# Kernel tuning notes

Measured on AMD Instinct MI355X. Metric: run time of the kernel, lower is better.

Reference implementation:

```python
import jax, jax.numpy as jnp
import numpy as np

N = 100000
E = 1600000
IN = 128
HID = 128
OUT = 64


def sage_conv(x, src, dst, deg_inv, W_l, b_l, W_r):
    # PyG SAGEConv (mean aggr): out = lin_l(mean_{j in N(i)} x_j) + lin_r(x_i)
    msgs = x[src]                                   # [E, F] gather
    agg = jax.ops.segment_sum(msgs, dst, num_segments=N)  # [N, F]
    agg = agg * deg_inv[:, None]                    # mean
    return agg @ W_l + b_l + x @ W_r


def setup_inputs() -> dict:
    key = jax.random.key(0)
    ks = jax.random.split(key, 9)
    x = jax.random.normal(ks[0], (N, IN), dtype=jnp.float32)
    edge_index = jax.random.randint(ks[1], (2, E), 0, N, dtype=jnp.int64)
    s = 1.0 / np.sqrt(IN)
    W1l = jax.random.uniform(ks[2], (IN, HID), jnp.float32, -s, s)
    b1 = jax.random.uniform(ks[3], (HID,), jnp.float32, -s, s)
    W1r = jax.random.uniform(ks[4], (IN, HID), jnp.float32, -s, s)
    s2 = 1.0 / np.sqrt(HID)
    W2l = jax.random.uniform(ks[5], (HID, HID), jnp.float32, -s2, s2)
    b2 = jax.random.uniform(ks[6], (HID,), jnp.float32, -s2, s2)
    W2r = jax.random.uniform(ks[7], (HID, HID), jnp.float32, -s2, s2)
    kl1, kl2 = jax.random.split(ks[8])
    Wlin = jax.random.uniform(kl1, (HID, OUT), jnp.float32, -s2, s2)
    blin = jax.random.uniform(kl2, (OUT,), jnp.float32, -s2, s2)
    return {"x": x, "edge_index": edge_index, "W1l": W1l, "b1": b1, "W1r": W1r,
            "W2l": W2l, "b2": b2, "W2r": W2r, "Wlin": Wlin, "blin": blin}


def reference(x, edge_index, W1l, b1, W1r, W2l, b2, W2r, Wlin, blin):
    src, dst = edge_index[0], edge_index[1]
    deg = jax.ops.segment_sum(jnp.ones((E,), jnp.float32), dst, num_segments=N)
    deg_inv = 1.0 / jnp.maximum(deg, 1.0)
    h = sage_conv(x, src, dst, deg_inv, W1l, b1, W1r)
    h = jax.nn.relu(h)
    # dropout: training=False -> identity
    h2 = sage_conv(h, src, dst, deg_inv, W2l, b2, W2r)
    h = jax.nn.relu(h + h2)
    return h @ Wlin + blin
```

## Files before the change

kernel.cpp:

```cpp
#include <hip/hip_runtime.h>
#include <hip/hip_bf16.h>
#include <cstdint>

#define NND 100000
#define NED 1600000
#define FIN 128
#define FOUT 64

#define NBLK 512
#define EPB (NED / NBLK)
#define NBUCK 256
#define BSH 9
#define BNODES 512
#define HTN (NBUCK * NBLK)

typedef __bf16 bf16x8 __attribute__((ext_vector_type(8)));
typedef float f32x4 __attribute__((ext_vector_type(4)));

static __device__ inline unsigned short f2bf(float f) {
    unsigned int u = __builtin_bit_cast(unsigned int, f);
    unsigned int r = (u + 0x7fffu + ((u >> 16) & 1u)) >> 16;
    return (unsigned short)r;
}
static __device__ inline float bflo(unsigned int v) {
    return __builtin_bit_cast(float, v << 16);
}
static __device__ inline float bfhi(unsigned int v) {
    return __builtin_bit_cast(float, v & 0xffff0000u);
}
static __device__ inline float bf1(unsigned short u) {
    return __builtin_bit_cast(float, (unsigned int)u << 16);
}

static __device__ inline void pack_one(const float* __restrict__ W,
                                       unsigned short* __restrict__ out,
                                       int NTtot, int c_local, int nt,
                                       int chunkOff, int ncols, int lane) {
    int k = c_local * 32 + (lane >> 4) * 8;
    int n = nt * 16 + (lane & 15);
    unsigned short t[8];
#pragma unroll
    for (int j = 0; j < 8; j++) t[j] = f2bf(W[(size_t)(k + j) * ncols + n]);
    uint4 u;
    u.x = t[0] | ((unsigned)t[1] << 16);
    u.y = t[2] | ((unsigned)t[3] << 16);
    u.z = t[4] | ((unsigned)t[5] << 16);
    u.w = t[6] | ((unsigned)t[7] << 16);
    *(uint4*)&out[((size_t)((c_local + chunkOff) * NTtot + nt) * 64 + lane) * 8] = u;
}

__global__ __launch_bounds__(256) void k_hist_cast(
        const int* __restrict__ dst, int* __restrict__ histT,
        const float* __restrict__ x, unsigned int* __restrict__ xb,
        const float* W1l, const float* W1r, const float* W2l,
        const float* W2r, const float* Wlin,
        unsigned short* p1, unsigned short* p2, unsigned short* ph) {
    __shared__ int hist[NBUCK];
    const int tid = threadIdx.x, blk = blockIdx.x;
    hist[tid] = 0;
    __syncthreads();
    const int e0 = blk * EPB, e1 = e0 + EPB;
    for (int i = e0 + tid; i < e1; i += 256)
        atomicAdd(&hist[dst[i] >> BSH], 1);
    __syncthreads();
    histT[tid * NBLK + blk] = hist[tid];
    if (blk < 144 && tid < 64) {
        int b = blk, lane = tid;
        if (b < 32)       pack_one(W1l, p1, 8, b >> 3, b & 7, 0, 128, lane);
        else if (b < 64)  { b -= 32; pack_one(W1r, p1, 8, b >> 3, b & 7, 4, 128, lane); }
        else if (b < 96)  { b -= 64; pack_one(W2l, p2, 8, b >> 3, b & 7, 0, 128, lane); }
        else if (b < 128) { b -= 96; pack_one(W2r, p2, 8, b >> 3, b & 7, 4, 128, lane); }
        else              { b -= 128; pack_one(Wlin, ph, 4, b >> 2, b & 3, 0, 64, lane); }
    }
    const int total2 = NND * 64;
    for (int i = blk * 256 + tid; i < total2; i += NBLK * 256) {
        float2 v = ((const float2*)x)[i];
        xb[i] = (unsigned int)f2bf(v.x) | ((unsigned int)f2bf(v.y) << 16);
    }
}

__global__ __launch_bounds__(1024) void g_scan1(const int* __restrict__ in,
                                                int* __restrict__ psum, int n) {
    __shared__ int red[1024];
    int tid = threadIdx.x;
    int i = blockIdx.x * 1024 + tid;
    red[tid] = (i < n) ? in[i] : 0;
    __syncthreads();
#pragma unroll
    for (int off = 512; off > 0; off >>= 1) {
        if (tid < off) red[tid] += red[tid + off];
        __syncthreads();
    }
    if (tid == 0) psum[blockIdx.x] = red[0];
}

__global__ __launch_bounds__(128) void g_scan2(int* __restrict__ psum, int nb) {
    int tid = threadIdx.x;
    int d = (tid < nb) ? psum[tid] : 0;
    int v = d;
#pragma unroll
    for (int off = 1; off < 64; off <<= 1) {
        int u = __shfl_up(v, off, 64);
        if ((tid & 63) >= off) v += u;
    }
    __shared__ int ws[2];
    if ((tid & 63) == 63) ws[tid >> 6] = v;
    __syncthreads();
    int base = (tid >= 64) ? ws[0] : 0;
    if (tid < nb) psum[tid] = base + v - d;
}

__global__ __launch_bounds__(1024) void g_scan3(const int* __restrict__ in,
                                                const int* __restrict__ psum,
                                                int* __restrict__ out, int n) {
    int tid = threadIdx.x;
    int i = blockIdx.x * 1024 + tid;
    int d = (i < n) ? in[i] : 0;
    int v = d;
#pragma unroll
    for (int off = 1; off < 64; off <<= 1) {
        int u = __shfl_up(v, off, 64);
        if ((tid & 63) >= off) v += u;
    }
    __shared__ int wsum[16];
    int wid = tid >> 6;
    if ((tid & 63) == 63) wsum[wid] = v;
    __syncthreads();
    if (tid < 16) {
        int w = wsum[tid];
#pragma unroll
        for (int off = 1; off < 16; off <<= 1) {
            int u = __shfl_up(w, off, 64);
            if (tid >= off) w += u;
        }
        wsum[tid] = w;
    }
    __syncthreads();
    int base = psum[blockIdx.x] + (wid ? wsum[wid - 1] : 0);
    if (i < n) out[i] = base + v - d;
}

__global__ __launch_bounds__(256) void k_scatter(const int* __restrict__ src,
                                                 const int* __restrict__ dst,
                                                 const int* __restrict__ sh,
                                                 uint2* __restrict__ eS) {
    __shared__ int cur[NBUCK];
    const int tid = threadIdx.x, blk = blockIdx.x;
    cur[tid] = sh[tid * NBLK + blk];
    __syncthreads();
    const int e0 = blk * EPB, e1 = e0 + EPB;
    for (int i = e0 + tid; i < e1; i += 256) {
        int d = dst[i];
        int pos = atomicAdd(&cur[d >> BSH], 1);
        eS[pos] = make_uint2((unsigned)src[i], (unsigned)(d & (BNODES - 1)));
    }
}

__global__ __launch_bounds__(1024) void k_bucket(const uint2* __restrict__ eS,
                                                 const int* __restrict__ sh,
                                                 int* __restrict__ csr,
                                                 int* __restrict__ offs,
                                                 float* __restrict__ dinv, int n) {
    __shared__ int cnt[BNODES];
    __shared__ int loc[BNODES];
    const int b = blockIdx.x, tid = threadIdx.x;
    const int base = sh[b * NBLK];
    const int end = (b == NBUCK - 1) ? NED : sh[(b + 1) * NBLK];
    if (tid < BNODES) cnt[tid] = 0;
    __syncthreads();
    for (int i = base + tid; i < end; i += 1024)
        atomicAdd(&cnt[eS[i].y], 1);
    __syncthreads();
    if (tid < BNODES) loc[tid] = cnt[tid];
    __syncthreads();
#pragma unroll
    for (int off = 1; off < BNODES; off <<= 1) {
        int v = 0;
        if (tid < BNODES && tid >= off) v = loc[tid - off];
        __syncthreads();
        if (tid < BNODES) loc[tid] += v;
        __syncthreads();
    }
    int node = b * BNODES + tid;
    int myExcl = 0;
    if (tid < BNODES) {
        myExcl = loc[tid] - cnt[tid];
        if (node < n) {
            offs[node] = base + myExcl;
            dinv[node] = 1.0f / fmaxf((float)cnt[tid], 1.0f);
        }
    }
    __syncthreads();
    if (tid < BNODES) cnt[tid] = base + myExcl;
    __syncthreads();
    for (int i = base + tid; i < end; i += 1024) {
        uint2 e = eS[i];
        int slot = atomicAdd(&cnt[e.y], 1);
        csr[slot] = (int)e.x;
    }
    if (b == 0 && tid == 0) offs[n] = NED;
}

#define ACC8(v) do { \
    acc[0].x += bflo((v).x); acc[0].y += bfhi((v).x); \
    acc[1].x += bflo((v).y); acc[1].y += bfhi((v).y); \
    acc[2].x += bflo((v).z); acc[2].y += bfhi((v).z); \
    acc[3].x += bflo((v).w); acc[3].y += bfhi((v).w); } while (0)

__global__ __launch_bounds__(256) void k_aggb(const uint4* __restrict__ feat4,
                                              const int* __restrict__ offs,
                                              const int* __restrict__ csr,
                                              const float* __restrict__ dinv,
                                              uint4* __restrict__ out4, int n) {
    int node = blockIdx.x * 4 + (threadIdx.x >> 6);
    if (node >= n) return;
    int lane = threadIdx.x & 63;
    int grp = lane >> 4;
    int ch = lane & 15;
    int beg = offs[node], end = offs[node + 1];
    int deg = end - beg;

    float2 acc[4];
#pragma unroll
    for (int j = 0; j < 4; j++) acc[j] = make_float2(0.f, 0.f);

    int i = beg;
    int fullEnd = beg + (deg & ~15);
    for (; i < fullEnd; i += 16) {
        int s0 = csr[i + grp];
        int s1 = csr[i + 4 + grp];
        int s2 = csr[i + 8 + grp];
        int s3 = csr[i + 12 + grp];
        uint4 v0 = feat4[(size_t)s0 * 16 + ch];
        uint4 v1 = feat4[(size_t)s1 * 16 + ch];
        uint4 v2 = feat4[(size_t)s2 * 16 + ch];
        uint4 v3 = feat4[(size_t)s3 * 16 + ch];
        ACC8(v0); ACC8(v1); ACC8(v2); ACC8(v3);
    }
    if (i < end) {
#pragma unroll
        for (int g = 0; g < 4; g++) {
            int e = i + g * 4 + grp;
            bool p = e < end;
            int s = csr[p ? e : beg];
            uint4 v = feat4[(size_t)s * 16 + ch];
            if (p) { ACC8(v); }
        }
    }
#pragma unroll
    for (int j = 0; j < 4; j++) {
        acc[j].x += __shfl_xor(acc[j].x, 16);
        acc[j].y += __shfl_xor(acc[j].y, 16);
        acc[j].x += __shfl_xor(acc[j].x, 32);
        acc[j].y += __shfl_xor(acc[j].y, 32);
    }
    if (grp == 0) {
        float di = dinv[node];
        uint4 o;
        o.x = (unsigned)f2bf(acc[0].x * di) | ((unsigned)f2bf(acc[0].y * di) << 16);
        o.y = (unsigned)f2bf(acc[1].x * di) | ((unsigned)f2bf(acc[1].y * di) << 16);
        o.z = (unsigned)f2bf(acc[2].x * di) | ((unsigned)f2bf(acc[2].y * di) << 16);
        o.w = (unsigned)f2bf(acc[3].x * di) | ((unsigned)f2bf(acc[3].y * di) << 16);
        out4[(size_t)node * 16 + ch] = o;
    }
}

template <int NT, int KCH, bool TWO, bool RELU, bool RESID, bool HEAD, bool OUTBF>
__global__ __launch_bounds__(256) void k_mfma(const unsigned short* __restrict__ P,
                                              const unsigned short* __restrict__ Q,
                                              const unsigned short* __restrict__ Wp,
                                              const float* __restrict__ bias,
                                              const unsigned short* __restrict__ resid,
                                              const unsigned short* __restrict__ Wp2,
                                              const float* __restrict__ bias2,
                                              void* __restrict__ outv, int n) {
    const int lane = threadIdx.x & 63;
    const int wave = threadIdx.x >> 6;
    const int quad = lane >> 4;
    const int row0 = blockIdx.x * 64 + wave * 16;
    int rowA = row0 + (lane & 15);
    if (rowA >= n) rowA = n - 1;

    f32x4 acc[NT];
#pragma unroll
    for (int t = 0; t < NT; t++) acc[t] = (f32x4){0.f, 0.f, 0.f, 0.f};

#pragma unroll
    for (int c = 0; c < KCH; c++) {
        const unsigned short* Abase = (TWO && c >= KCH / 2) ? Q : P;
        const int kk = (TWO ? (c & (KCH / 2 - 1)) : c) * 32 + quad * 8;
        bf16x8 a = *(const bf16x8*)&Abase[(size_t)rowA * 128 + kk];
#pragma unroll
        for (int t = 0; t < NT; t++) {
            bf16x8 b = *(const bf16x8*)&Wp[(size_t)((c * NT + t) * 64 + lane) * 8];
            acc[t] = __builtin_amdgcn_mfma_f32_16x16x32_bf16(a, b, acc[t], 0, 0, 0);
        }
    }

    const int col = lane & 15;
    if (!HEAD) {
#pragma unroll
        for (int t = 0; t < NT; t++) {
            float bv = bias[t * 16 + col];
#pragma unroll
            for (int r = 0; r < 4; r++) {
                int row = row0 + quad * 4 + r;
                if (row < n) {
                    float v = acc[t][r] + bv;
                    if (RESID) v += bf1(resid[(size_t)row * 128 + t * 16 + col]);
                    if (RELU) v = fmaxf(v, 0.f);
                    if (OUTBF)
                        ((unsigned short*)outv)[(size_t)row * (NT * 16) + t * 16 + col] = f2bf(v);
                    else
                        ((float*)outv)[(size_t)row * (NT * 16) + t * 16 + col] = v;
                }
            }
        }
    } else {
        __shared__ __align__(16) unsigned short sT[4][16 * 136];
#pragma unroll
        for (int t = 0; t < NT; t++) {
            float bv = bias[t * 16 + col];
#pragma unroll
            for (int r = 0; r < 4; r++) {
                int row = row0 + quad * 4 + r;
                int rr = row < n ? row : n - 1;
                float v = acc[t][r] + bv;
                if (RESID) v += bf1(resid[(size_t)rr * 128 + t * 16 + col]);
                if (RELU) v = fmaxf(v, 0.f);
                sT[wave][(quad * 4 + r) * 136 + t * 16 + col] = f2bf(v);
            }
        }
        f32x4 hacc[4];
#pragma unroll
        for (int t = 0; t < 4; t++) hacc[t] = (f32x4){0.f, 0.f, 0.f, 0.f};
#pragma unroll
        for (int c = 0; c < 4; c++) {
            bf16x8 a = *(const bf16x8*)&sT[wave][(lane & 15) * 136 + c * 32 + quad * 8];
#pragma unroll
            for (int t = 0; t < 4; t++) {
                bf16x8 b = *(const bf16x8*)&Wp2[(size_t)((c * 4 + t) * 64 + lane) * 8];
                hacc[t] = __builtin_amdgcn_mfma_f32_16x16x32_bf16(a, b, hacc[t], 0, 0, 0);
            }
        }
#pragma unroll
        for (int t = 0; t < 4; t++) {
            float bv = bias2[t * 16 + col];
#pragma unroll
            for (int r = 0; r < 4; r++) {
                int row = row0 + quad * 4 + r;
                if (row < n)
                    ((float*)outv)[(size_t)row * 64 + t * 16 + col] = hacc[t][r] + bv;
            }
        }
    }
}

extern "C" void kernel_launch(void* const* d_in, const int* in_sizes, int n_in,
                              void* d_out, int out_size, void* d_ws, size_t ws_size,
                              hipStream_t stream) {
    const float* x    = (const float*)d_in[0];
    const int*   ei   = (const int*)d_in[1];
    const float* W1l  = (const float*)d_in[2];
    const float* b1   = (const float*)d_in[3];
    const float* W1r  = (const float*)d_in[4];
    const float* W2l  = (const float*)d_in[5];
    const float* b2   = (const float*)d_in[6];
    const float* W2r  = (const float*)d_in[7];
    const float* Wlin = (const float*)d_in[8];
    const float* blin = (const float*)d_in[9];
    float* out = (float*)d_out;

    const int N = NND, E = NED;
    const int* src = ei;
    const int* dst = ei + E;
    const int NB2 = HTN / 1024;

    char* w = (char*)d_ws;
    int*   histT  = (int*)w;               w += (size_t)HTN * 4;
    int*   sh     = (int*)w;               w += (size_t)HTN * 4;
    int*   psum   = (int*)w;               w += (size_t)NB2 * 4;
    int*   offs   = (int*)w;               w += (size_t)(N + 4) * 4;
    float* dinv   = (float*)w;             w += (size_t)N * 4;
    uint2* eS     = (uint2*)w;             w += (size_t)E * 8;
    int*   csr    = (int*)w;               w += (size_t)E * 4;
    unsigned short* p1  = (unsigned short*)w;  w += 256 * 128 * 2;
    unsigned short* p2  = (unsigned short*)w;  w += 256 * 128 * 2;
    unsigned short* ph  = (unsigned short*)w;  w += 128 * 64 * 2;
    unsigned short* xb  = (unsigned short*)w;  w += (size_t)N * 128 * 2;
    unsigned short* agg = (unsigned short*)w;  w += (size_t)N * 128 * 2;
    unsigned short* h1  = (unsigned short*)w;  w += (size_t)N * 128 * 2;

    k_hist_cast<<<NBLK, 256, 0, stream>>>(dst, histT, x, (unsigned int*)xb,
                                          W1l, W1r, W2l, W2r, Wlin, p1, p2, ph);
    g_scan1<<<NB2, 1024, 0, stream>>>(histT, psum, HTN);
    g_scan2<<<1, 128, 0, stream>>>(psum, NB2);
    g_scan3<<<NB2, 1024, 0, stream>>>(histT, psum, sh, HTN);
    k_scatter<<<NBLK, 256, 0, stream>>>(src, dst, sh, eS);
    k_bucket<<<NBUCK, 1024, 0, stream>>>(eS, sh, csr, offs, dinv, N);

    k_aggb<<<(N + 3) / 4, 256, 0, stream>>>((const uint4*)xb, offs, csr, dinv,
                                            (uint4*)agg, N);
    k_mfma<8, 8, true, true, false, false, true><<<(N + 63) / 64, 256, 0, stream>>>(
        agg, xb, p1, b1, nullptr, nullptr, nullptr, h1, N);

    k_aggb<<<(N + 3) / 4, 256, 0, stream>>>((const uint4*)h1, offs, csr, dinv,
                                            (uint4*)agg, N);
    k_mfma<8, 8, true, true, true, true, false><<<(N + 63) / 64, 256, 0, stream>>>(
        agg, h1, p2, b2, h1, ph, blin, out, N);
}
```

Before: 388.3 us.

## Fuse neighbor aggregation into MFMA linear kernel and pack edge keys

Merges the per-node mean aggregation and the dense SAGE linear layer into one kernel. Aggregated rows are staged in LDS instead of going through a global bf16 buffer, which removes the write and reread of that intermediate and two launches. The bucket-sort edge records are packed into 32-bit words (local node in the high bits, source in the low 20), and the histogram block count drops from 512 to 256. In exchange, each fused block does serial gathers for 16 nodes per wave before any MFMA work, so there are fewer blocks and less latency hiding for the irregular gathers.

New measurement: 445.9 us. 1.15x slower.

```diff
diff --git a/kernel.cpp b/kernel.cpp
--- a/kernel.cpp
+++ b/kernel.cpp
@@ -7,7 +7,7 @@
 #define FIN 128
 #define FOUT 64
 
-#define NBLK 512
+#define NBLK 256
 #define EPB (NED / NBLK)
 #define NBUCK 256
 #define BSH 9
@@ -143,7 +143,7 @@
 __global__ __launch_bounds__(256) void k_scatter(const int* __restrict__ src,
                                                  const int* __restrict__ dst,
                                                  const int* __restrict__ sh,
-                                                 uint2* __restrict__ eS) {
+                                                 unsigned int* __restrict__ eS) {
     __shared__ int cur[NBUCK];
     const int tid = threadIdx.x, blk = blockIdx.x;
     cur[tid] = sh[tid * NBLK + blk];
@@ -152,11 +152,11 @@
     for (int i = e0 + tid; i < e1; i += 256) {
         int d = dst[i];
         int pos = atomicAdd(&cur[d >> BSH], 1);
-        eS[pos] = make_uint2((unsigned)src[i], (unsigned)(d & (BNODES - 1)));
-    }
-}
-
-__global__ __launch_bounds__(1024) void k_bucket(const uint2* __restrict__ eS,
+        eS[pos] = ((unsigned)(d & (BNODES - 1)) << 20) | (unsigned)src[i];
+    }
+}
+
+__global__ __launch_bounds__(1024) void k_bucket(const unsigned int* __restrict__ eS,
                                                  const int* __restrict__ sh,
                                                  int* __restrict__ csr,
                                                  int* __restrict__ offs,
@@ -169,7 +169,7 @@
     if (tid < BNODES) cnt[tid] = 0;
     __syncthreads();
     for (int i = base + tid; i < end; i += 1024)
-        atomicAdd(&cnt[eS[i].y], 1);
+        atomicAdd(&cnt[eS[i] >> 20], 1);
     __syncthreads();
     if (tid < BNODES) loc[tid] = cnt[tid];
     __syncthreads();
@@ -194,9 +194,9 @@
     if (tid < BNODES) cnt[tid] = base + myExcl;
     __syncthreads();
     for (int i = base + tid; i < end; i += 1024) {
-        uint2 e = eS[i];
-        int slot = atomicAdd(&cnt[e.y], 1);
-        csr[slot] = (int)e.x;
+        unsigned int e = eS[i];
+        int slot = atomicAdd(&cnt[e >> 20], 1);
+        csr[slot] = (int)(e & 0xFFFFFu);
     }
     if (b == 0 && tid == 0) offs[n] = NED;
 }
@@ -207,127 +207,125 @@
     acc[2].x += bflo((v).z); acc[2].y += bfhi((v).z); \
     acc[3].x += bflo((v).w); acc[3].y += bfhi((v).w); } while (0)
 
-__global__ __launch_bounds__(256) void k_aggb(const uint4* __restrict__ feat4,
-                                              const int* __restrict__ offs,
-                                              const int* __restrict__ csr,
-                                              const float* __restrict__ dinv,
-                                              uint4* __restrict__ out4, int n) {
-    int node = blockIdx.x * 4 + (threadIdx.x >> 6);
-    if (node >= n) return;
-    int lane = threadIdx.x & 63;
-    int grp = lane >> 4;
-    int ch = lane & 15;
-    int beg = offs[node], end = offs[node + 1];
-    int deg = end - beg;
-
-    float2 acc[4];
-#pragma unroll
-    for (int j = 0; j < 4; j++) acc[j] = make_float2(0.f, 0.f);
-
-    int i = beg;
-    int fullEnd = beg + (deg & ~15);
-    for (; i < fullEnd; i += 16) {
-        int s0 = csr[i + grp];
-        int s1 = csr[i + 4 + grp];
-        int s2 = csr[i + 8 + grp];
-        int s3 = csr[i + 12 + grp];
-        uint4 v0 = feat4[(size_t)s0 * 16 + ch];
-        uint4 v1 = feat4[(size_t)s1 * 16 + ch];
-        uint4 v2 = feat4[(size_t)s2 * 16 + ch];
-        uint4 v3 = feat4[(size_t)s3 * 16 + ch];
-        ACC8(v0); ACC8(v1); ACC8(v2); ACC8(v3);
-    }
-    if (i < end) {
-#pragma unroll
-        for (int g = 0; g < 4; g++) {
-            int e = i + g * 4 + grp;
-            bool p = e < end;
-            int s = csr[p ? e : beg];
-            uint4 v = feat4[(size_t)s * 16 + ch];
-            if (p) { ACC8(v); }
-        }
-    }
-#pragma unroll
-    for (int j = 0; j < 4; j++) {
-        acc[j].x += __shfl_xor(acc[j].x, 16);
-        acc[j].y += __shfl_xor(acc[j].y, 16);
-        acc[j].x += __shfl_xor(acc[j].x, 32);
-        acc[j].y += __shfl_xor(acc[j].y, 32);
-    }
-    if (grp == 0) {
-        float di = dinv[node];
-        uint4 o;
-        o.x = (unsigned)f2bf(acc[0].x * di) | ((unsigned)f2bf(acc[0].y * di) << 16);
-        o.y = (unsigned)f2bf(acc[1].x * di) | ((unsigned)f2bf(acc[1].y * di) << 16);
-        o.z = (unsigned)f2bf(acc[2].x * di) | ((unsigned)f2bf(acc[2].y * di) << 16);
-        o.w = (unsigned)f2bf(acc[3].x * di) | ((unsigned)f2bf(acc[3].y * di) << 16);
-        out4[(size_t)node * 16 + ch] = o;
-    }
-}
-
-template <int NT, int KCH, bool TWO, bool RELU, bool RESID, bool HEAD, bool OUTBF>
-__global__ __launch_bounds__(256) void k_mfma(const unsigned short* __restrict__ P,
-                                              const unsigned short* __restrict__ Q,
-                                              const unsigned short* __restrict__ Wp,
-                                              const float* __restrict__ bias,
-                                              const unsigned short* __restrict__ resid,
-                                              const unsigned short* __restrict__ Wp2,
-                                              const float* __restrict__ bias2,
-                                              void* __restrict__ outv, int n) {
-    const int lane = threadIdx.x & 63;
-    const int wave = threadIdx.x >> 6;
+template <bool RESID, bool HEAD, bool OUTBF>
+__global__ __launch_bounds__(256) void k_agg_mfma(
+        const uint4* __restrict__ feat4,
+        const unsigned short* __restrict__ Q,
+        const int* __restrict__ offs, const int* __restrict__ csr,
+        const float* __restrict__ dinv,
+        const unsigned short* __restrict__ Wp, const float* __restrict__ bias,
+        const unsigned short* __restrict__ Wp2, const float* __restrict__ bias2,
+        void* __restrict__ outv, int n) {
+    const int tid = threadIdx.x;
+    const int lane = tid & 63, wave = tid >> 6;
+    const int grp = lane >> 4, ch = lane & 15;
+    const int row0 = blockIdx.x * 64;
+
+    __shared__ __align__(16) unsigned short sAgg[64 * 136];
+
+    for (int nn = 0; nn < 16; nn++) {
+        int node = row0 + wave * 16 + nn;
+        int nd = node < n ? node : n - 1;
+        int beg = offs[nd], end = offs[nd + 1];
+        int deg = end - beg;
+        float2 acc[4];
+#pragma unroll
+        for (int j = 0; j < 4; j++) acc[j] = make_float2(0.f, 0.f);
+        int i = beg;
+        int fullEnd = beg + (deg & ~15);
+        for (; i < fullEnd; i += 16) {
+            int s0 = csr[i + grp];
+            int s1 = csr[i + 4 + grp];
+            int s2 = csr[i + 8 + grp];
+            int s3 = csr[i + 12 + grp];
+            uint4 v0 = feat4[(size_t)s0 * 16 + ch];
+            uint4 v1 = feat4[(size_t)s1 * 16 + ch];
+            uint4 v2 = feat4[(size_t)s2 * 16 + ch];
+            uint4 v3 = feat4[(size_t)s3 * 16 + ch];
+            ACC8(v0); ACC8(v1); ACC8(v2); ACC8(v3);
+        }
+        if (i < end) {
+#pragma unroll
+            for (int g = 0; g < 4; g++) {
+                int e = i + g * 4 + grp;
+                bool p = e < end;
+                int s = csr[p ? e : beg];
+                uint4 v = feat4[(size_t)s * 16 + ch];
+                if (p) { ACC8(v); }
+            }
+        }
+#pragma unroll
+        for (int j = 0; j < 4; j++) {
+            acc[j].x += __shfl_xor(acc[j].x, 16);
+            acc[j].y += __shfl_xor(acc[j].y, 16);
+            acc[j].x += __shfl_xor(acc[j].x, 32);
+            acc[j].y += __shfl_xor(acc[j].y, 32);
+        }
+        if (grp == 0) {
+            float di = dinv[nd];
+            uint4 o;
+            o.x = (unsigned)f2bf(acc[0].x * di) | ((unsigned)f2bf(acc[0].y * di) << 16);
+            o.y = (unsigned)f2bf(acc[1].x * di) | ((unsigned)f2bf(acc[1].y * di) << 16);
+            o.z = (unsigned)f2bf(acc[2].x * di) | ((unsigned)f2bf(acc[2].y * di) << 16);
+            o.w = (unsigned)f2bf(acc[3].x * di) | ((unsigned)f2bf(acc[3].y * di) << 16);
+            *(uint4*)&sAgg[(wave * 16 + nn) * 136 + ch * 8] = o;
+        }
+    }
+
     const int quad = lane >> 4;
-    const int row0 = blockIdx.x * 64 + wave * 16;
-    int rowA = row0 + (lane & 15);
-    if (rowA >= n) rowA = n - 1;
-
-    f32x4 acc[NT];
-#pragma unroll
-    for (int t = 0; t < NT; t++) acc[t] = (f32x4){0.f, 0.f, 0.f, 0.f};
-
-#pragma unroll
-    for (int c = 0; c < KCH; c++) {
-        const unsigned short* Abase = (TWO && c >= KCH / 2) ? Q : P;
-        const int kk = (TWO ? (c & (KCH / 2 - 1)) : c) * 32 + quad * 8;
-        bf16x8 a = *(const bf16x8*)&Abase[(size_t)rowA * 128 + kk];
-#pragma unroll
-        for (int t = 0; t < NT; t++) {
-            bf16x8 b = *(const bf16x8*)&Wp[(size_t)((c * NT + t) * 64 + lane) * 8];
-            acc[t] = __builtin_amdgcn_mfma_f32_16x16x32_bf16(a, b, acc[t], 0, 0, 0);
+    const int m = lane & 15;
+    int rowA = row0 + wave * 16 + m;
+    int rowAc = rowA < n ? rowA : n - 1;
+
+    f32x4 macc[8];
+#pragma unroll
+    for (int t = 0; t < 8; t++) macc[t] = (f32x4){0.f, 0.f, 0.f, 0.f};
+
+#pragma unroll
+    for (int c = 0; c < 8; c++) {
+        bf16x8 a;
+        if (c < 4)
+            a = *(const bf16x8*)&sAgg[(wave * 16 + m) * 136 + c * 32 + quad * 8];
+        else
+            a = *(const bf16x8*)&Q[(size_t)rowAc * 128 + (c - 4) * 32 + quad * 8];
+#pragma unroll
+        for (int t = 0; t < 8; t++) {
+            bf16x8 b = *(const bf16x8*)&Wp[(size_t)((c * 8 + t) * 64 + lane) * 8];
+            macc[t] = __builtin_amdgcn_mfma_f32_16x16x32_bf16(a, b, macc[t], 0, 0, 0);
         }
     }
 
     const int col = lane & 15;
     if (!HEAD) {
 #pragma unroll
-        for (int t = 0; t < NT; t++) {
+        for (int t = 0; t < 8; t++) {
             float bv = bias[t * 16 + col];
 #pragma unroll
             for (int r = 0; r < 4; r++) {
-                int row = row0 + quad * 4 + r;
+                int row = row0 + wave * 16 + quad * 4 + r;
                 if (row < n) {
-                    float v = acc[t][r] + bv;
-                    if (RESID) v += bf1(resid[(size_t)row * 128 + t * 16 + col]);
-                    if (RELU) v = fmaxf(v, 0.f);
+                    float v = macc[t][r] + bv;
+                    if (RESID) v += bf1(Q[(size_t)row * 128 + t * 16 + col]);
+                    v = fmaxf(v, 0.f);
                     if (OUTBF)
-                        ((unsigned short*)outv)[(size_t)row * (NT * 16) + t * 16 + col] = f2bf(v);
+                        ((unsigned short*)outv)[(size_t)row * 128 + t * 16 + col] = f2bf(v);
                     else
-                        ((float*)outv)[(size_t)row * (NT * 16) + t * 16 + col] = v;
+                        ((float*)outv)[(size_t)row * 128 + t * 16 + col] = v;
                 }
             }
         }
     } else {
         __shared__ __align__(16) unsigned short sT[4][16 * 136];
 #pragma unroll
-        for (int t = 0; t < NT; t++) {
+        for (int t = 0; t < 8; t++) {
             float bv = bias[t * 16 + col];
 #pragma unroll
             for (int r = 0; r < 4; r++) {
-                int row = row0 + quad * 4 + r;
+                int row = row0 + wave * 16 + quad * 4 + r;
                 int rr = row < n ? row : n - 1;
-                float v = acc[t][r] + bv;
-                if (RESID) v += bf1(resid[(size_t)rr * 128 + t * 16 + col]);
-                if (RELU) v = fmaxf(v, 0.f);
+                float v = macc[t][r] + bv;
+                if (RESID) v += bf1(Q[(size_t)rr * 128 + t * 16 + col]);
+                v = fmaxf(v, 0.f);
                 sT[wave][(quad * 4 + r) * 136 + t * 16 + col] = f2bf(v);
             }
         }
@@ -336,7 +334,7 @@
         for (int t = 0; t < 4; t++) hacc[t] = (f32x4){0.f, 0.f, 0.f, 0.f};
 #pragma unroll
         for (int c = 0; c < 4; c++) {
-            bf16x8 a = *(const bf16x8*)&sT[wave][(lane & 15) * 136 + c * 32 + quad * 8];
+            bf16x8 a = *(const bf16x8*)&sT[wave][m * 136 + c * 32 + quad * 8];
 #pragma unroll
             for (int t = 0; t < 4; t++) {
                 bf16x8 b = *(const bf16x8*)&Wp2[(size_t)((c * 4 + t) * 64 + lane) * 8];
@@ -348,7 +346,7 @@
             float bv = bias2[t * 16 + col];
 #pragma unroll
             for (int r = 0; r < 4; r++) {
-                int row = row0 + quad * 4 + r;
+                int row = row0 + wave * 16 + quad * 4 + r;
                 if (row < n)
                     ((float*)outv)[(size_t)row * 64 + t * 16 + col] = hacc[t][r] + bv;
             }
@@ -382,13 +380,12 @@
     int*   psum   = (int*)w;               w += (size_t)NB2 * 4;
     int*   offs   = (int*)w;               w += (size_t)(N + 4) * 4;
     float* dinv   = (float*)w;             w += (size_t)N * 4;
-    uint2* eS     = (uint2*)w;             w += (size_t)E * 8;
+    unsigned int* eS = (unsigned int*)w;   w += (size_t)E * 4;
     int*   csr    = (int*)w;               w += (size_t)E * 4;
     unsigned short* p1  = (unsigned short*)w;  w += 256 * 128 * 2;
     unsigned short* p2  = (unsigned short*)w;  w += 256 * 128 * 2;
     unsigned short* ph  = (unsigned short*)w;  w += 128 * 64 * 2;
     unsigned short* xb  = (unsigned short*)w;  w += (size_t)N * 128 * 2;
-    unsigned short* agg = (unsigned short*)w;  w += (size_t)N * 128 * 2;
     unsigned short* h1  = (unsigned short*)w;  w += (size_t)N * 128 * 2;
 
     k_hist_cast<<<NBLK, 256, 0, stream>>>(dst, histT, x, (unsigned int*)xb,
@@ -399,13 +396,9 @@
     k_scatter<<<NBLK, 256, 0, stream>>>(src, dst, sh, eS);
     k_bucket<<<NBUCK, 1024, 0, stream>>>(eS, sh, csr, offs, dinv, N);
 
-    k_aggb<<<(N + 3) / 4, 256, 0, stream>>>((const uint4*)xb, offs, csr, dinv,
-                                            (uint4*)agg, N);
-    k_mfma<8, 8, true, true, false, false, true><<<(N + 63) / 64, 256, 0, stream>>>(
-        agg, xb, p1, b1, nullptr, nullptr, nullptr, h1, N);
-
-    k_aggb<<<(N + 3) / 4, 256, 0, stream>>>((const uint4*)h1, offs, csr, dinv,
-                                            (uint4*)agg, N);
-    k_mfma<8, 8, true, true, true, true, false><<<(N + 63) / 64, 256, 0, stream>>>(
-        agg, h1, p2, b2, h1, ph, blin, out, N);
-}
+    k_agg_mfma<false, false, true><<<(N + 63) / 64, 256, 0, stream>>>(
+        (const uint4*)xb, xb, offs, csr, dinv, p1, b1, nullptr, nullptr, h1, N);
+
+    k_agg_mfma<true, true, false><<<(N + 63) / 64, 256, 0, stream>>>(
+        (const uint4*)h1, h1, offs, csr, dinv, p2, b2, ph, blin, out, N);
+}
```
